# Kernel optimization log

Hardware: AMD Instinct MI355X
Metric: run time of the kernel (lower is better)

## Reference

```python
import jax, jax.numpy as jnp
import numpy as np

N, D = 4096, 128  # seq length / feature dim of x is N; head dim is D

def setup_inputs() -> dict:
    key = jax.random.key(0)
    k1, k2 = jax.random.split(key)
    x = jax.random.normal(k1, (N, N), dtype=jnp.float32)
    # nn.Linear(N, 3*d): weight [3d, N], bias [3d]; scale weight like torch init
    W = jax.random.normal(k2, (3 * D, N), dtype=jnp.float32) / jnp.sqrt(jnp.float32(N))
    b = jnp.zeros((3 * D,), dtype=jnp.float32)
    return {"x": x, "W": W, "b": b}

def reference(x, W, b):
    # QKV projection: [N, 3d]
    qkv = x @ W.T + b
    Q, K, V = jnp.split(qkv, 3, axis=-1)  # each [N, d]
    # The blockwise online-softmax double loop computes exactly
    # softmax(Q K^T) V with NO 1/sqrt(d) scaling (faithful to source).
    S = Q @ K.T                 # [N, N]
    P = jax.nn.softmax(S, axis=-1)
    return P @ V                # [N, d]
```

## Files before the change

kernel.cpp:

```cpp
#include <hip/hip_runtime.h>
#include <cstdint>
#include <cstddef>

typedef _Float16 f16;
typedef f16 f16x8 __attribute__((ext_vector_type(8)));
typedef f16 f16x4 __attribute__((ext_vector_type(4)));
typedef float f32x4 __attribute__((ext_vector_type(4)));

#define SEQ 4096
#define DH 128
#define QKV_LD 384
#define LOG2E 1.44269504f

__device__ __forceinline__ float fast_exp2(float x) {
#if __has_builtin(__builtin_amdgcn_exp2f)
  return __builtin_amdgcn_exp2f(x);
#else
  return exp2f(x);
#endif
}

template <int CTRL>
__device__ __forceinline__ float dppf(float x) {
  int r = __builtin_amdgcn_mov_dpp(__builtin_bit_cast(int, x), CTRL, 0xF, 0xF, true);
  return __builtin_bit_cast(float, r);
}
__device__ __forceinline__ float rmax16(float v) {
  v = fmaxf(v, dppf<0x128>(v));
  v = fmaxf(v, dppf<0x124>(v));
  v = fmaxf(v, dppf<0x4E>(v));
  v = fmaxf(v, dppf<0xB1>(v));
  return v;
}
__device__ __forceinline__ float rsum16(float v) {
  v += dppf<0x128>(v);
  v += dppf<0x124>(v);
  v += dppf<0x4E>(v);
  v += dppf<0xB1>(v);
  return v;
}

__global__ __launch_bounds__(256) void cvt_w_kernel(const float4* __restrict__ W,
                                                    f16x4* __restrict__ Wh) {
  int i = blockIdx.x * 256 + threadIdx.x;
  float4 v = W[i];
  f16x4 h; h[0] = (f16)v.x; h[1] = (f16)v.y; h[2] = (f16)v.z; h[3] = (f16)v.w;
  Wh[i] = h;
}

template <int SPLITS>
__global__ __launch_bounds__(256, 2) void gemm_qkv(const float* __restrict__ x,
                                                   const f16* __restrict__ Wh,
                                                   f16* __restrict__ part) {
  __shared__ f16 Ax[64][72];
  __shared__ f16 Bx[384][72];
  const int m0 = blockIdx.x * 64;
  const int split = blockIdx.y;
  const int k0 = split * (SEQ / SPLITS);
  const int tid = threadIdx.x;
  const int lane = tid & 63, wave = tid >> 6;
  const int nb = wave * 96;
  const int l15 = lane & 15, quad = lane >> 4;

  f32x4 acc[4][6] = {};

  for (int kt = k0; kt < k0 + SEQ / SPLITS; kt += 64) {
#pragma unroll
    for (int r = 0; r < 4; ++r) {
      int c = tid + r * 256;
      int row = c >> 4, col = (c & 15) * 4;
      float4 v = *(const float4*)&x[(size_t)(m0 + row) * SEQ + kt + col];
      f16x4 h; h[0] = (f16)v.x; h[1] = (f16)v.y; h[2] = (f16)v.z; h[3] = (f16)v.w;
      *(f16x4*)&Ax[row][col] = h;
    }
#pragma unroll
    for (int r = 0; r < 12; ++r) {
      int c = tid + r * 256;
      int row = c >> 3, col = (c & 7) * 8;
      *(f16x8*)&Bx[row][col] = *(const f16x8*)&Wh[(size_t)row * SEQ + kt + col];
    }
    __syncthreads();
#pragma unroll
    for (int ks = 0; ks < 2; ++ks) {
      f16x8 a[4], bb[6];
#pragma unroll
      for (int t = 0; t < 4; ++t)
        a[t] = *(const f16x8*)&Ax[t * 16 + l15][ks * 32 + quad * 8];
#pragma unroll
      for (int t = 0; t < 6; ++t)
        bb[t] = *(const f16x8*)&Bx[nb + t * 16 + l15][ks * 32 + quad * 8];
#pragma unroll
      for (int mt = 0; mt < 4; ++mt)
#pragma unroll
        for (int nt = 0; nt < 6; ++nt)
          acc[mt][nt] = __builtin_amdgcn_mfma_f32_16x16x32_f16(a[mt], bb[nt], acc[mt][nt], 0, 0, 0);
    }
    __syncthreads();
  }

  f16* pw = part + (size_t)split * SEQ * QKV_LD;
#pragma unroll
  for (int mt = 0; mt < 4; ++mt) {
#pragma unroll
    for (int nt = 0; nt < 6; ++nt) {
      int col = nb + nt * 16 + l15;
      int rowbase = m0 + mt * 16 + quad * 4;
#pragma unroll
      for (int rr = 0; rr < 4; ++rr)
        pw[(size_t)(rowbase + rr) * QKV_LD + col] = (f16)acc[mt][nt][rr];
    }
  }
}

template <int SPLITS>
__global__ __launch_bounds__(256) void reduce_qkv(const f16* __restrict__ part,
                                                  const float* __restrict__ bias,
                                                  f16* __restrict__ qkv) {
  int i = (blockIdx.x * 256 + threadIdx.x) * 8;
  float acc[8] = {};
#pragma unroll
  for (int s = 0; s < SPLITS; ++s) {
    f16x8 p = *(const f16x8*)&part[(size_t)s * SEQ * QKV_LD + i];
#pragma unroll
    for (int j = 0; j < 8; ++j) acc[j] += (float)p[j];
  }
  int col = i % QKV_LD;
  f16x8 o;
#pragma unroll
  for (int j = 0; j < 8; ++j) o[j] = (f16)(acc[j] + bias[col + j]);
  *(f16x8*)&qkv[i] = o;
}

__global__ __launch_bounds__(256) void transpose_v(const f16* __restrict__ qkv,
                                                   f16* __restrict__ Vt) {
  __shared__ f16 T[64][72];
  const int r0 = blockIdx.x * 64;
  const int c0 = blockIdx.y * 64;
  const int tid = threadIdx.x;
#pragma unroll
  for (int rep = 0; rep < 2; ++rep) {
    int idx = rep * 256 + tid;
    int row = idx >> 3, col = (idx & 7) * 8;
    *(f16x8*)&T[row][col] = *(const f16x8*)&qkv[(size_t)(r0 + row) * QKV_LD + 256 + c0 + col];
  }
  __syncthreads();
#pragma unroll
  for (int rep = 0; rep < 2; ++rep) {
    int idx = rep * 256 + tid;
    int cc = idx >> 3, rb = (idx & 7) * 8;
    f16x8 o;
#pragma unroll
    for (int j = 0; j < 8; ++j) o[j] = T[rb + j][cc];
    *(f16x8*)&Vt[(size_t)(c0 + cc) * SEQ + r0 + rb] = o;
  }
}

#define NSPLIT 16
#define KVRANGE (SEQ / NSPLIT)

__global__ __launch_bounds__(256, 2) void attn_partial(const f16* __restrict__ qkv,
                                                       const f16* __restrict__ Vt,
                                                       f16* __restrict__ Op,
                                                       float* __restrict__ ml) {
  __shared__ f16 Ks[64][136];
  __shared__ f16 Vs[128][72];
  __shared__ f16 Pt[4][64][36];

  const int q0 = blockIdx.x * 128;
  const int split = blockIdx.y;
  const int kv0 = split * KVRANGE;
  const int tid = threadIdx.x;
  const int lane = tid & 63, wave = tid >> 6;
  const int l15 = lane & 15, quad = lane >> 4;
  const int mbase = q0 + wave * 32;

  f16x8 qf[2][4];
#pragma unroll
  for (int mt = 0; mt < 2; ++mt)
#pragma unroll
    for (int ks = 0; ks < 4; ++ks) {
      f16x8 q = *(const f16x8*)&qkv[(size_t)(mbase + mt * 16 + l15) * QKV_LD + ks * 32 + quad * 8];
      qf[mt][ks] = q * (f16)LOG2E;
    }

  f32x4 oacc[2][8] = {};
  float mrow[2][4], lrow[2][4];
#pragma unroll
  for (int mt = 0; mt < 2; ++mt)
#pragma unroll
    for (int rr = 0; rr < 4; ++rr) { mrow[mt][rr] = -1e30f; lrow[mt][rr] = 0.f; }

  for (int it = 0; it < KVRANGE / 64; ++it) {
    const int k0 = kv0 + it * 64;
#pragma unroll
    for (int r = 0; r < 4; ++r) {
      int c = tid + r * 256;
      int row = c >> 4, col = (c & 15) * 8;
      *(f16x8*)&Ks[row][col] = *(const f16x8*)&qkv[(size_t)(k0 + row) * QKV_LD + DH + col];
    }
#pragma unroll
    for (int r = 0; r < 4; ++r) {
      int c = tid + r * 256;
      int row = c >> 3, col = (c & 7) * 8;
      *(f16x8*)&Vs[row][col] = *(const f16x8*)&Vt[(size_t)row * SEQ + k0 + col];
    }
    __syncthreads();

    f32x4 s[2][4] = {};
#pragma unroll
    for (int ks = 0; ks < 4; ++ks) {
      f16x8 kf[4];
#pragma unroll
      for (int nt = 0; nt < 4; ++nt)
        kf[nt] = *(const f16x8*)&Ks[nt * 16 + l15][ks * 32 + quad * 8];
#pragma unroll
      for (int mt = 0; mt < 2; ++mt)
#pragma unroll
        for (int nt = 0; nt < 4; ++nt)
          s[mt][nt] = __builtin_amdgcn_mfma_f32_16x16x32_f16(qf[mt][ks], kf[nt], s[mt][nt], 0, 0, 0);
    }

#pragma unroll
    for (int mt = 0; mt < 2; ++mt) {
      float mnew[4], al[4];
#pragma unroll
      for (int rr = 0; rr < 4; ++rr) {
        float v = fmaxf(fmaxf(s[mt][0][rr], s[mt][1][rr]), fmaxf(s[mt][2][rr], s[mt][3][rr]));
        v = rmax16(v);
        mnew[rr] = fmaxf(mrow[mt][rr], v);
        al[rr] = fast_exp2(mrow[mt][rr] - mnew[rr]);
        mrow[mt][rr] = mnew[rr];
      }
      float ls[4] = {0.f, 0.f, 0.f, 0.f};
#pragma unroll
      for (int nt = 0; nt < 4; ++nt) {
        f16x4 pk;
#pragma unroll
        for (int rr = 0; rr < 4; ++rr) {
          float p = fast_exp2(s[mt][nt][rr] - mnew[rr]);
          ls[rr] += p;
          pk[rr] = (f16)p;
        }
        *(f16x4*)&Pt[wave][nt * 16 + l15][mt * 16 + quad * 4] = pk;
      }
#pragma unroll
      for (int rr = 0; rr < 4; ++rr)
        lrow[mt][rr] = lrow[mt][rr] * al[rr] + rsum16(ls[rr]);
#pragma unroll
      for (int dt = 0; dt < 8; ++dt)
#pragma unroll
        for (int rr = 0; rr < 4; ++rr)
          oacc[mt][dt][rr] *= al[rr];
    }
    __syncthreads();

#pragma unroll
    for (int kk = 0; kk < 2; ++kk) {
      f16x8 pf[2];
#pragma unroll
      for (int mt = 0; mt < 2; ++mt)
#pragma unroll
        for (int j = 0; j < 8; ++j)
          pf[mt][j] = Pt[wave][kk * 32 + quad * 8 + j][mt * 16 + l15];
#pragma unroll
      for (int dt = 0; dt < 8; ++dt) {
        f16x8 vf = *(const f16x8*)&Vs[dt * 16 + l15][kk * 32 + quad * 8];
        oacc[0][dt] = __builtin_amdgcn_mfma_f32_16x16x32_f16(pf[0], vf, oacc[0][dt], 0, 0, 0);
        oacc[1][dt] = __builtin_amdgcn_mfma_f32_16x16x32_f16(pf[1], vf, oacc[1][dt], 0, 0, 0);
      }
    }
    __syncthreads();
  }

#pragma unroll
  for (int mt = 0; mt < 2; ++mt) {
#pragma unroll
    for (int dt = 0; dt < 8; ++dt)
#pragma unroll
      for (int rr = 0; rr < 4; ++rr) {
        int row = mbase + mt * 16 + quad * 4 + rr;
        Op[((size_t)split * SEQ + row) * DH + dt * 16 + l15] = (f16)oacc[mt][dt][rr];
      }
    if (l15 == 0) {
#pragma unroll
      for (int rr = 0; rr < 4; ++rr) {
        int row = mbase + mt * 16 + quad * 4 + rr;
        ml[((size_t)split * SEQ + row) * 2 + 0] = mrow[mt][rr];
        ml[((size_t)split * SEQ + row) * 2 + 1] = lrow[mt][rr];
      }
    }
  }
}

__global__ __launch_bounds__(256) void combine_kernel(const f16* __restrict__ Op,
                                                      const float* __restrict__ ml,
                                                      float* __restrict__ out) {
  int idx = blockIdx.x * 256 + threadIdx.x;
  int row = idx >> 7;
  float ms[NSPLIT], ls[NSPLIT];
  float M = -1e30f;
#pragma unroll
  for (int s = 0; s < NSPLIT; ++s) {
    ms[s] = ml[((size_t)s * SEQ + row) * 2 + 0];
    ls[s] = ml[((size_t)s * SEQ + row) * 2 + 1];
    M = fmaxf(M, ms[s]);
  }
  float L = 0.f, o = 0.f;
#pragma unroll
  for (int s = 0; s < NSPLIT; ++s) {
    float w = fast_exp2(ms[s] - M);
    L += ls[s] * w;
    o += w * (float)Op[(size_t)s * SEQ * DH + idx];
  }
  out[idx] = o / L;
}

extern "C" void kernel_launch(void* const* d_in, const int* in_sizes, int n_in,
                              void* d_out, int out_size, void* d_ws, size_t ws_size,
                              hipStream_t stream) {
  const float* x = (const float*)d_in[0];
  const float* W = (const float*)d_in[1];
  const float* b = (const float*)d_in[2];
  float* out = (float*)d_out;
  char* ws = (char*)d_ws;

  f16*   Wh   = (f16*)(ws);
  f16*   qkv  = (f16*)(ws + (3u << 20));
  f16*   Vt   = (f16*)(ws + (6u << 20));
  float* ml   = (float*)(ws + (7u << 20));
  char*  scr  = ws + (7u << 20) + (1u << 19);
  f16*   part = (f16*)scr;
  f16*   Op   = (f16*)scr;

  cvt_w_kernel<<<(384 * 4096 / 4) / 256, 256, 0, stream>>>((const float4*)W, (f16x4*)Wh);

  bool big = ws_size >= ((size_t)31u << 20) + ((size_t)1u << 19);
  if (big) {
    gemm_qkv<8><<<dim3(SEQ / 64, 8), 256, 0, stream>>>(x, Wh, part);
    reduce_qkv<8><<<SEQ * QKV_LD / 8 / 256, 256, 0, stream>>>(part, b, qkv);
  } else {
    gemm_qkv<4><<<dim3(SEQ / 64, 4), 256, 0, stream>>>(x, Wh, part);
    reduce_qkv<4><<<SEQ * QKV_LD / 8 / 256, 256, 0, stream>>>(part, b, qkv);
  }
  transpose_v<<<dim3(SEQ / 64, DH / 64), 256, 0, stream>>>(qkv, Vt);
  attn_partial<<<dim3(SEQ / 128, NSPLIT), 256, 0, stream>>>(qkv, Vt, Op, ml);
  combine_kernel<<<(SEQ * DH) / 256, 256, 0, stream>>>(Op, ml, out);
}
```

Measured before the change: 154.5 us.

## Swap QK^T operand order, direct-to-LDS weight loads with XOR swizzle

```diff
diff --git a/kernel.cpp b/kernel.cpp
--- a/kernel.cpp
+++ b/kernel.cpp
@@ -20,24 +20,9 @@
 #endif
 }
 
-template <int CTRL>
-__device__ __forceinline__ float dppf(float x) {
-  int r = __builtin_amdgcn_mov_dpp(__builtin_bit_cast(int, x), CTRL, 0xF, 0xF, true);
-  return __builtin_bit_cast(float, r);
-}
-__device__ __forceinline__ float rmax16(float v) {
-  v = fmaxf(v, dppf<0x128>(v));
-  v = fmaxf(v, dppf<0x124>(v));
-  v = fmaxf(v, dppf<0x4E>(v));
-  v = fmaxf(v, dppf<0xB1>(v));
-  return v;
-}
-__device__ __forceinline__ float rsum16(float v) {
-  v += dppf<0x128>(v);
-  v += dppf<0x124>(v);
-  v += dppf<0x4E>(v);
-  v += dppf<0xB1>(v);
-  return v;
+__device__ __forceinline__ void gl_lds16(const void* g, void* l) {
+  __builtin_amdgcn_global_load_lds((const __attribute__((address_space(1))) void*)g,
+                                   (__attribute__((address_space(3))) void*)l, 16, 0, 0);
 }
 
 __global__ __launch_bounds__(256) void cvt_w_kernel(const float4* __restrict__ W,
@@ -52,33 +37,36 @@
 __global__ __launch_bounds__(256, 2) void gemm_qkv(const float* __restrict__ x,
                                                    const f16* __restrict__ Wh,
                                                    f16* __restrict__ part) {
-  __shared__ f16 Ax[64][72];
-  __shared__ f16 Bx[384][72];
+  __shared__ __align__(16) f16 Ax[64][72];
+  __shared__ __align__(16) f16 Bx[QKV_LD * 64];
   const int m0 = blockIdx.x * 64;
   const int split = blockIdx.y;
-  const int k0 = split * (SEQ / SPLITS);
+  const int kc = SEQ / SPLITS;
+  const int k0 = split * kc;
   const int tid = threadIdx.x;
-  const int lane = tid & 63, wave = tid >> 6;
+  const int lane = tid & 63;
+  const int wave = tid >> 6;
   const int nb = wave * 96;
   const int l15 = lane & 15, quad = lane >> 4;
 
   f32x4 acc[4][6] = {};
 
-  for (int kt = k0; kt < k0 + SEQ / SPLITS; kt += 64) {
+  for (int kt = k0; kt < k0 + kc; kt += 64) {
+#pragma unroll
+    for (int r = 0; r < 12; ++r) {
+      int c = r * 256 + tid;
+      int row = c >> 3, ch = c & 7;
+      const f16* src = &Wh[(size_t)row * SEQ + kt + ((ch ^ (row & 7)) << 3)];
+      gl_lds16(src, &Bx[(size_t)c << 3]);
+    }
 #pragma unroll
     for (int r = 0; r < 4; ++r) {
-      int c = tid + r * 256;
+      int c = r * 256 + tid;
       int row = c >> 4, col = (c & 15) * 4;
       float4 v = *(const float4*)&x[(size_t)(m0 + row) * SEQ + kt + col];
       f16x4 h; h[0] = (f16)v.x; h[1] = (f16)v.y; h[2] = (f16)v.z; h[3] = (f16)v.w;
       *(f16x4*)&Ax[row][col] = h;
     }
-#pragma unroll
-    for (int r = 0; r < 12; ++r) {
-      int c = tid + r * 256;
-      int row = c >> 3, col = (c & 7) * 8;
-      *(f16x8*)&Bx[row][col] = *(const f16x8*)&Wh[(size_t)row * SEQ + kt + col];
-    }
     __syncthreads();
 #pragma unroll
     for (int ks = 0; ks < 2; ++ks) {
@@ -87,8 +75,11 @@
       for (int t = 0; t < 4; ++t)
         a[t] = *(const f16x8*)&Ax[t * 16 + l15][ks * 32 + quad * 8];
 #pragma unroll
-      for (int t = 0; t < 6; ++t)
-        bb[t] = *(const f16x8*)&Bx[nb + t * 16 + l15][ks * 32 + quad * 8];
+      for (int t = 0; t < 6; ++t) {
+        int n = nb + t * 16 + l15;
+        int ch = (ks * 4 + quad) ^ (l15 & 7);
+        bb[t] = *(const f16x8*)&Bx[((size_t)n << 6) + (ch << 3)];
+      }
 #pragma unroll
       for (int mt = 0; mt < 4; ++mt)
 #pragma unroll
@@ -133,7 +124,7 @@
 
 __global__ __launch_bounds__(256) void transpose_v(const f16* __restrict__ qkv,
                                                    f16* __restrict__ Vt) {
-  __shared__ f16 T[64][72];
+  __shared__ __align__(16) f16 T[64][72];
   const int r0 = blockIdx.x * 64;
   const int c0 = blockIdx.y * 64;
   const int tid = threadIdx.x;
@@ -162,9 +153,9 @@
                                                        const f16* __restrict__ Vt,
                                                        f16* __restrict__ Op,
                                                        float* __restrict__ ml) {
-  __shared__ f16 Ks[64][136];
-  __shared__ f16 Vs[128][72];
-  __shared__ f16 Pt[4][64][36];
+  __shared__ __align__(16) f16 Ks[64][136];
+  __shared__ __align__(16) f16 Vs[128][72];
+  __shared__ __align__(16) f16 Ps[4][32][72];
 
   const int q0 = blockIdx.x * 128;
   const int split = blockIdx.y;
@@ -184,11 +175,8 @@
     }
 
   f32x4 oacc[2][8] = {};
-  float mrow[2][4], lrow[2][4];
-#pragma unroll
-  for (int mt = 0; mt < 2; ++mt)
-#pragma unroll
-    for (int rr = 0; rr < 4; ++rr) { mrow[mt][rr] = -1e30f; lrow[mt][rr] = 0.f; }
+  float mrow[2] = {-1e30f, -1e30f};
+  float lrow[2] = {0.f, 0.f};
 
   for (int it = 0; it < KVRANGE / 64; ++it) {
     const int k0 = kv0 + it * 64;
@@ -206,74 +194,83 @@
     }
     __syncthreads();
 
-    f32x4 s[2][4] = {};
+    f32x4 st[4][2] = {};
 #pragma unroll
     for (int ks = 0; ks < 4; ++ks) {
       f16x8 kf[4];
 #pragma unroll
-      for (int nt = 0; nt < 4; ++nt)
-        kf[nt] = *(const f16x8*)&Ks[nt * 16 + l15][ks * 32 + quad * 8];
-#pragma unroll
-      for (int mt = 0; mt < 2; ++mt)
-#pragma unroll
-        for (int nt = 0; nt < 4; ++nt)
-          s[mt][nt] = __builtin_amdgcn_mfma_f32_16x16x32_f16(qf[mt][ks], kf[nt], s[mt][nt], 0, 0, 0);
-    }
-
+      for (int kt = 0; kt < 4; ++kt)
+        kf[kt] = *(const f16x8*)&Ks[kt * 16 + l15][ks * 32 + quad * 8];
+#pragma unroll
+      for (int kt = 0; kt < 4; ++kt)
+#pragma unroll
+        for (int mt = 0; mt < 2; ++mt)
+          st[kt][mt] = __builtin_amdgcn_mfma_f32_16x16x32_f16(kf[kt], qf[mt][ks], st[kt][mt], 0, 0, 0);
+    }
+
+    float al[2];
 #pragma unroll
     for (int mt = 0; mt < 2; ++mt) {
-      float mnew[4], al[4];
-#pragma unroll
-      for (int rr = 0; rr < 4; ++rr) {
-        float v = fmaxf(fmaxf(s[mt][0][rr], s[mt][1][rr]), fmaxf(s[mt][2][rr], s[mt][3][rr]));
-        v = rmax16(v);
-        mnew[rr] = fmaxf(mrow[mt][rr], v);
-        al[rr] = fast_exp2(mrow[mt][rr] - mnew[rr]);
-        mrow[mt][rr] = mnew[rr];
-      }
-      float ls[4] = {0.f, 0.f, 0.f, 0.f};
-#pragma unroll
-      for (int nt = 0; nt < 4; ++nt) {
+      float v = -1e30f;
+#pragma unroll
+      for (int kt = 0; kt < 4; ++kt)
+#pragma unroll
+        for (int rr = 0; rr < 4; ++rr) v = fmaxf(v, st[kt][mt][rr]);
+      v = fmaxf(v, __shfl_xor(v, 16));
+      v = fmaxf(v, __shfl_xor(v, 32));
+      float mnew = fmaxf(mrow[mt], v);
+      al[mt] = fast_exp2(mrow[mt] - mnew);
+      mrow[mt] = mnew;
+      float ls = 0.f;
+#pragma unroll
+      for (int kt = 0; kt < 4; ++kt) {
         f16x4 pk;
 #pragma unroll
         for (int rr = 0; rr < 4; ++rr) {
-          float p = fast_exp2(s[mt][nt][rr] - mnew[rr]);
-          ls[rr] += p;
+          float p = fast_exp2(st[kt][mt][rr] - mnew);
+          ls += p;
           pk[rr] = (f16)p;
         }
-        *(f16x4*)&Pt[wave][nt * 16 + l15][mt * 16 + quad * 4] = pk;
+        *(f16x4*)&Ps[wave][mt * 16 + l15][kt * 16 + quad * 4] = pk;
       }
+      ls += __shfl_xor(ls, 16);
+      ls += __shfl_xor(ls, 32);
+      lrow[mt] = lrow[mt] * al[mt] + ls;
+    }
+
+    float alr[2][4];
+#pragma unroll
+    for (int mt = 0; mt < 2; ++mt)
 #pragma unroll
       for (int rr = 0; rr < 4; ++rr)
-        lrow[mt][rr] = lrow[mt][rr] * al[rr] + rsum16(ls[rr]);
+        alr[mt][rr] = __shfl(al[mt], quad * 4 + rr);
+#pragma unroll
+    for (int mt = 0; mt < 2; ++mt)
 #pragma unroll
       for (int dt = 0; dt < 8; ++dt)
 #pragma unroll
         for (int rr = 0; rr < 4; ++rr)
-          oacc[mt][dt][rr] *= al[rr];
-    }
-    __syncthreads();
+          oacc[mt][dt][rr] *= alr[mt][rr];
 
 #pragma unroll
     for (int kk = 0; kk < 2; ++kk) {
       f16x8 pf[2];
 #pragma unroll
       for (int mt = 0; mt < 2; ++mt)
-#pragma unroll
-        for (int j = 0; j < 8; ++j)
-          pf[mt][j] = Pt[wave][kk * 32 + quad * 8 + j][mt * 16 + l15];
+        pf[mt] = *(const f16x8*)&Ps[wave][mt * 16 + l15][kk * 32 + quad * 8];
 #pragma unroll
       for (int dt = 0; dt < 8; ++dt) {
         f16x8 vf = *(const f16x8*)&Vs[dt * 16 + l15][kk * 32 + quad * 8];
-        oacc[0][dt] = __builtin_amdgcn_mfma_f32_16x16x32_f16(pf[0], vf, oacc[0][dt], 0, 0, 0);
-        oacc[1][dt] = __builtin_amdgcn_mfma_f32_16x16x32_f16(pf[1], vf, oacc[1][dt], 0, 0, 0);
+#pragma unroll
+        for (int mt = 0; mt < 2; ++mt)
+          oacc[mt][dt] = __builtin_amdgcn_mfma_f32_16x16x32_f16(pf[mt], vf, oacc[mt][dt], 0, 0, 0);
       }
     }
     __syncthreads();
   }
 
 #pragma unroll
-  for (int mt = 0; mt < 2; ++mt) {
+  for (int mt = 0; mt < 2; ++mt)
 #pragma unroll
     for (int dt = 0; dt < 8; ++dt)
 #pragma unroll
@@ -281,13 +278,12 @@
         int row = mbase + mt * 16 + quad * 4 + rr;
         Op[((size_t)split * SEQ + row) * DH + dt * 16 + l15] = (f16)oacc[mt][dt][rr];
       }
-    if (l15 == 0) {
-#pragma unroll
-      for (int rr = 0; rr < 4; ++rr) {
-        int row = mbase + mt * 16 + quad * 4 + rr;
-        ml[((size_t)split * SEQ + row) * 2 + 0] = mrow[mt][rr];
-        ml[((size_t)split * SEQ + row) * 2 + 1] = lrow[mt][rr];
-      }
+  if (quad == 0) {
+#pragma unroll
+    for (int mt = 0; mt < 2; ++mt) {
+      int row = mbase + mt * 16 + l15;
+      ml[((size_t)split * SEQ + row) * 2 + 0] = mrow[mt];
+      ml[((size_t)split * SEQ + row) * 2 + 1] = lrow[mt];
     }
   }
 }
```

Result: no change. 152.0 us (-1.7%).
